# Optimization experiments

Measured on AMD Instinct MI355X. Metric: run time of the kernel, lower is better.

## Reference

```python
import jax, jax.numpy as jnp
import numpy as np

B, T, H, A = 16, 6000, 256, 1
NOTE_CLS = 104            # note_num + 4
NOTE_NUM, NOTE_START = 100, 30
THRESHOLD = 0.5
MIN_GAP = 9


def conv1d(x, w, b):
    # x: [B,T,C], w: [K,Cin,Cout] (kernel 3, padding 1 == SAME)
    return jax.lax.conv_general_dilated(x, w, (1,), 'SAME', dimension_numbers=('NWC', 'WIO', 'NWC')) + b


def layer_norm(x, g, b, eps=1e-5):
    m = jnp.mean(x, -1, keepdims=True)
    v = jnp.mean((x - m) ** 2, -1, keepdims=True)
    return (x - m) * jax.lax.rsqrt(v + eps) * g + b


def regulate_boundary(bd_logits, non_padding):
    # threshold -> per-run local argmax -> min-gap NMS merge, sequential per row
    probs = jax.nn.sigmoid(bd_logits)          # [B,T]
    bd = probs > THRESHOLD
    Tn = probs.shape[1]

    def one_row(bd_i, p_i):
        def step(carry, j):
            res, start, last, best_i, best_v = carry
            is_one, pj = bd_i[j], p_i[j]
            opening = is_one & (start < 0)
            # running argmax over current run (first-occurrence tie-break like torch.argmax)
            upd = opening | (is_one & (start >= 0) & (pj > best_v))
            best_i = jnp.where(upd, j, best_i)
            best_v = jnp.where(upd, pj, best_v)
            start = jnp.where(opening, j, start)
            close = (~is_one) & (start >= 0)
            merge = close & ((best_i - last) < MIN_GAP) & (last > 0)
            # Python round() / half-to-even, matches round((bd_idx+last)/2)
            mid = jnp.round((best_i + last).astype(jnp.float32) * 0.5).astype(jnp.int32)
            final_idx = jnp.where(merge, mid, best_i)
            res = res.at[last].set(jnp.where(merge, 0, res[last]))
            res = res.at[final_idx].set(jnp.where(close, 1, res[final_idx]))
            last = jnp.where(close, final_idx, last)
            start = jnp.where(close, jnp.int32(-1), start)
            return (res, start, last, best_i, best_v), None

        init = (jnp.zeros((Tn,), jnp.int32), jnp.int32(-1), jnp.int32(-1), jnp.int32(0), jnp.float32(-1e30))
        (res, *_), _ = jax.lax.scan(step, init, jnp.arange(Tn, dtype=jnp.int32))
        return res

    res = jax.vmap(one_row)(bd, probs)
    res = res.at[:, 0].set(0)
    lens = non_padding.sum(1)                  # bd_res[i, sum(non_padding[i])-1:] = 0
    res = jnp.where(jnp.arange(Tn)[None, :] >= (lens - 1)[:, None], 0, res)
    return res


def setup_inputs() -> dict:
    key = jax.random.key(0)
    ks = jax.random.split(key, 16)
    s = 1.0 / np.sqrt(H)
    return {
        'feat': jax.random.normal(ks[0], (B, T, H), jnp.float32),
        'non_padding': jnp.ones((B, T), jnp.int32),
        'w_bd': jax.random.normal(ks[1], (H, 1), jnp.float32) * s,
        'b_bd': jnp.zeros((1,), jnp.float32),
        'w_attn': jax.random.normal(ks[2], (H, A), jnp.float32) * s,
        'b_attn': jnp.zeros((A,), jnp.float32),
        'conv_w': jax.random.normal(ks[3], (3, H, H), jnp.float32) * s,
        'conv_b': jnp.zeros((H,), jnp.float32),
        'ln_g': jnp.ones((H,), jnp.float32),
        'ln_b': jnp.zeros((H,), jnp.float32),
        'post_w': jax.random.normal(ks[4], (3, H, H), jnp.float32) * s,
        'post_b': jnp.zeros((H,), jnp.float32),
        'w_pitch': jax.random.normal(ks[5], (H, NOTE_CLS), jnp.float32) * s,
        'b_pitch': jnp.zeros((NOTE_CLS,), jnp.float32),
    }


def reference(feat, non_padding, w_bd, b_bd, w_attn, b_attn, conv_w, conv_b, ln_g, ln_b, post_w, post_b, w_pitch, b_pitch):
    # note boundary logits (note_bd_out, temperature 1, clamp)
    note_bd_logits = jnp.clip((feat @ w_bd + b_bd)[..., 0], -16.0, 16.0)      # [B,T]
    note_bd = regulate_boundary(note_bd_logits, non_padding)                  # [B,T] int

    # --- PitchDecoder ---
    attn = jax.nn.sigmoid(feat @ w_attn + b_attn)                             # [B,T,A]
    attn_mean = attn.mean(-1)                                                 # [B,T]
    # mean over heads of feat[...,None]*attn[:,:,None,:] == feat * mean(attn)
    attn_feat = feat * attn_mean[..., None]                                   # [B,T,H]
    mel2note = jnp.cumsum(note_bd, axis=1)                                    # [B,T]
    note_lengths = note_bd.sum(axis=1) + 1
    N = feat.shape[1] + 1                                                     # static upper bound on note_length
    seg = jax.vmap(lambda d, s2: jax.ops.segment_sum(d, s2, num_segments=N))
    denom = seg(attn_mean, mel2note)                                          # [B,N]
    agg = seg(attn_feat, mel2note) / (denom[..., None] + 1e-5)                # [B,N,H]
    # post ConvBlocks (1 residual conv layer + post conv, kernel 3, leakyrelu)
    h = jax.nn.leaky_relu(layer_norm(conv1d(agg, conv_w, conv_b), ln_g, ln_b), 0.01)
    agg = conv1d(agg + h, post_w, post_b)
    note_logits = agg @ w_pitch + b_pitch                                     # [B,N,104]
    note_pred = jnp.argmax(note_logits, axis=-1)
    note_pred = jnp.where((note_pred > NOTE_NUM) | (note_pred < NOTE_START), 0, note_pred)
    return note_bd_logits, note_bd, note_lengths, note_logits, note_pred
```

## Files before the change

kernel.cpp:

```cpp
#include <hip/hip_runtime.h>
#include <math.h>

#define B 16
#define T 6000
#define H 256
#define NPOS 6001
#define NOTE_CLS 104
#define NOTE_NUM 100
#define NOTE_START 30
#define MIN_GAP 9
#define SEGC 384

#define T2 16
#define NT2 ((NPOS + T2 - 1) / T2)
#define CT 4
#define NCT (SEGC / CT)
#define ZSTR 260

#define NWORDS 94
#define MAXRUNS 3088

__global__ __launch_bounds__(256) void k_dots(
    const float* __restrict__ feat,
    const float* __restrict__ w_bd, const float* __restrict__ b_bd,
    const float* __restrict__ w_attn, const float* __restrict__ b_attn,
    float* __restrict__ out_logits, double* __restrict__ dlog,
    float* __restrict__ amean)
{
  int lane = threadIdx.x & 63, wv = threadIdx.x >> 6;
  int row = blockIdx.x * 4 + wv;
  if (row >= B * T) return;
  float4 f  = ((const float4*)(feat + (size_t)row * H))[lane];
  float4 wb = ((const float4*)w_bd)[lane];
  float4 wa = ((const float4*)w_attn)[lane];
  double sb = (double)f.x * wb.x + (double)f.y * wb.y + (double)f.z * wb.z + (double)f.w * wb.w;
  double sa = (double)f.x * wa.x + (double)f.y * wa.y + (double)f.z * wa.z + (double)f.w * wa.w;
  for (int off = 32; off; off >>= 1) { sb += __shfl_down(sb, off); sa += __shfl_down(sa, off); }
  if (lane == 0) {
    double lb = sb + (double)b_bd[0];
    lb = fmin(fmax(lb, -16.0), 16.0);
    out_logits[row] = (float)lb;
    dlog[row] = lb;
    double la = sa + (double)b_attn[0];
    amean[row] = (float)(1.0 / (1.0 + exp(-la)));
  }
}

__device__ __forceinline__ int block_scan_excl(int* a, int n, int tid, int lane,
                                               int wv, int* wsums)
{
  int base = 0;
  for (int c0 = 0; c0 < n; c0 += 256) {
    int i = c0 + tid;
    int v = (i < n) ? a[i] : 0;
    int s = v;
    #pragma unroll
    for (int off = 1; off < 64; off <<= 1) {
      int t = __shfl_up(s, off);
      if (lane >= off) s += t;
    }
    if (lane == 63) wsums[wv] = s;
    __syncthreads();
    int wbase = 0;
    for (int w = 0; w < wv; ++w) wbase += wsums[w];
    int ctot = wsums[0] + wsums[1] + wsums[2] + wsums[3];
    if (i < n) a[i] = base + wbase + s - v;
    base += ctot;
    __syncthreads();
  }
  return base;
}

__global__ __launch_bounds__(256) void k_regulate(
    const double* __restrict__ dlog, const int* __restrict__ non_padding,
    float* __restrict__ out_bd, float* __restrict__ out_len,
    int* __restrict__ seg_start, int* __restrict__ note_len)
{
  __shared__ double row_s[T];
  __shared__ unsigned long long words[96];
  __shared__ unsigned long long smask[NWORDS], emask[NWORDS];
  __shared__ int wcnt[NWORDS], woff[NWORDS], ecnt[NWORDS], eoff[NWORDS];
  __shared__ int starts_s[MAXRUNS];
  __shared__ int ends_s[MAXRUNS];
  __shared__ int besti_s[MAXRUNS];
  __shared__ int cstart_s[MAXRUNS + 1];
  __shared__ int kofs_s[MAXRUNS];
  __shared__ unsigned long long cmask[52];
  __shared__ int ccnt[52], coff[52];
  __shared__ int wsums[4], red_i[4];
  __shared__ int R_s, NC_s, lens_s;

  int b = blockIdx.x, tid = threadIdx.x;
  int lane = tid & 63, wv = tid >> 6;
  const double* row = dlog + (size_t)b * T;

  for (int c = 0; c < 24; ++c) {
    int t = c * 256 + tid;
    double d = (t < T) ? row[t] : -1.0;
    if (t < T) row_s[t] = d;
    unsigned long long m = __ballot((t < T) && (d > 0.0));
    if (lane == 0) words[c * 4 + wv] = m;
  }
  __syncthreads();

  if (tid < NWORDS) {
    unsigned long long bits = words[tid];
    unsigned long long carry = (tid > 0) ? (words[tid - 1] >> 63) : 0ull;
    unsigned long long pm = (bits << 1) | carry;
    unsigned long long sm = bits & ~pm;
    unsigned long long em = (~bits) & pm;
    smask[tid] = sm;  emask[tid] = em;
    wcnt[tid] = __popcll(sm);  ecnt[tid] = __popcll(em);
  }
  __syncthreads();

  if (tid == 0) {
    int a = 0, e = 0;
    #pragma unroll 8
    for (int w = 0; w < NWORDS; ++w) {
      woff[w] = a; a += wcnt[w];
      eoff[w] = e; e += ecnt[w];
    }
    R_s = a;
  }
  __syncthreads();

  if (tid < NWORDS) {
    unsigned long long m = smask[tid];
    int off = woff[tid], base = tid * 64;
    while (m) { int i = __builtin_ctzll(m); starts_s[off++] = base + i; m &= m - 1; }
    m = emask[tid]; off = eoff[tid];
    while (m) { int i = __builtin_ctzll(m); ends_s[off++] = base + i; m &= m - 1; }
  }

  {
    int lens = 0;
    const int* npr = non_padding + (size_t)b * T;
    for (int t = tid; t < T; t += 256) lens += npr[t];
    for (int off = 32; off; off >>= 1) lens += __shfl_down(lens, off);
    if (lane == 0) red_i[wv] = lens;
  }
  __syncthreads();
  if (tid == 0) lens_s = red_i[0] + red_i[1] + red_i[2] + red_i[3];

  int R = R_s;
  int bd_last = (int)((words[(T - 1) >> 6] >> ((T - 1) & 63)) & 1ull);
  int Rc = R - (bd_last ? 1 : 0);

  for (int r = tid; r < R; r += 256) {
    int s = starts_s[r];
    int e = (r < Rc) ? ends_s[r] : T;
    double bv = row_s[s];
    int bi = s;
    for (int t = s + 1; t < e; ++t) {
      double d = row_s[t];
      if (d > bv) { bv = d; bi = t; }
    }
    besti_s[r] = bi;
  }
  __syncthreads();

  int NRW = (Rc + 63) >> 6;
  for (int c0 = 0; c0 < NRW * 64; c0 += 256) {
    int r = c0 + tid;
    bool fl = false;
    if (r < Rc) fl = (r == 0) || (besti_s[r] - besti_s[r - 1] >= MIN_GAP);
    unsigned long long m = __ballot(fl);
    int widx = (c0 >> 6) + wv;
    if (lane == 0 && widx < 52) cmask[widx] = m;
  }
  __syncthreads();
  if (tid < NRW) ccnt[tid] = __popcll(cmask[tid]);
  __syncthreads();
  if (tid == 0) {
    int a = 0;
    for (int w = 0; w < NRW; ++w) { coff[w] = a; a += ccnt[w]; }
    NC_s = a;
  }
  __syncthreads();
  if (tid < NRW) {
    unsigned long long m = cmask[tid];
    int off = coff[tid], base = tid * 64;
    while (m) { int i = __builtin_ctzll(m); cstart_s[off++] = base + i; m &= m - 1; }
  }
  __syncthreads();
  int NC = NC_s;
  if (tid == 0) cstart_s[NC] = Rc;
  __syncthreads();

  for (int j = tid; j < NC; j += 256) {
    int r0 = cstart_s[j], r1 = cstart_s[j + 1];
    int last = -1, kc = 0;
    for (int r = r0; r < r1; ++r) {
      int bi = besti_s[r];
      bool merge = (last > 0) && (bi - last < MIN_GAP);
      int fi = bi;
      if (merge) { int sm2 = bi + last; fi = (sm2 + ((sm2 >> 1) & 1)) >> 1; }
      if (merge) besti_s[r0 + kc - 1] = fi;
      else       besti_s[r0 + kc++]   = fi;
      last = fi;
    }
    kofs_s[j] = kc;
  }
  __syncthreads();

  int K = block_scan_excl(kofs_s, NC, tid, lane, wv, wsums);
  __syncthreads();
  for (int j = tid; j < NC; j += 256) {
    int off = kofs_s[j];
    int cnt = ((j + 1 < NC) ? kofs_s[j + 1] : K) - off;
    int src = cstart_s[j];
    for (int k = 0; k < cnt; ++k) starts_s[off + k] = besti_s[src + k];
  }
  __syncthreads();

  int lens = lens_s;
  for (int i = tid; i < K; i += 256) {
    int e = starts_s[i];
    ends_s[i] = (e != 0 && e < lens - 1) ? 1 : 0;
  }
  __syncthreads();
  int keep = block_scan_excl(ends_s, K, tid, lane, wv, wsums);

  float* obd = out_bd + (size_t)b * T;
  for (int t = tid; t < T; t += 256) obd[t] = 0.f;
  __syncthreads();
  int* ss = seg_start + b * (T + 2);
  for (int i = tid; i < K; i += 256) {
    int e = starts_s[i];
    if (e != 0 && e < lens - 1) {
      int pos = ends_s[i];
      ss[pos + 1] = e;
      obd[e] = 1.f;
    }
  }
  if (tid == 0) {
    ss[0] = 0;
    ss[keep + 1] = T;
    note_len[b] = keep + 1;
    out_len[b] = (float)(keep + 1);
  }
}

__global__ __launch_bounds__(256) void k_consts(
    const float* __restrict__ conv_b, const float* __restrict__ ln_g,
    const float* __restrict__ ln_b, const float* __restrict__ post_w,
    const float* __restrict__ post_b, const float* __restrict__ w_pitch,
    const float* __restrict__ b_pitch,
    float* __restrict__ lmid, float* __restrict__ ledge, int* __restrict__ preds)
{
  __shared__ float hc[H], zm[H], ze[H], red[8];
  __shared__ float lm[NOTE_CLS], le[NOTE_CLS];
  int tid = threadIdx.x, lane = tid & 63, wv = tid >> 6;
  float y = conv_b[tid];
  float s = y;
  for (int off = 32; off; off >>= 1) s += __shfl_down(s, off);
  if (lane == 0) red[wv] = s;
  __syncthreads();
  float mean = (red[0] + red[1] + red[2] + red[3]) * (1.0f / H);
  float d = y - mean, q = d * d;
  for (int off = 32; off; off >>= 1) q += __shfl_down(q, off);
  if (lane == 0) red[4 + wv] = q;
  __syncthreads();
  float var = (red[4] + red[5] + red[6] + red[7]) * (1.0f / H);
  float h = d / sqrtf(var + 1e-5f) * ln_g[tid] + ln_b[tid];
  h = h > 0.f ? h : 0.01f * h;
  hc[tid] = h;
  __syncthreads();
  float am = 0.f, ae = 0.f;
  for (int cin = 0; cin < H; ++cin) {
    float hv = hc[cin];
    float p0 = post_w[(0 * H + cin) * H + tid];
    float p1 = post_w[(1 * H + cin) * H + tid];
    float p2 = post_w[(2 * H + cin) * H + tid];
    am += (p0 + p1 + p2) * hv;
    ae += (p0 + p1) * hv;
  }
  zm[tid] = am + post_b[tid];
  ze[tid] = ae + post_b[tid];
  __syncthreads();
  if (tid < NOTE_CLS) {
    float sm = 0.f, se = 0.f;
    for (int c = 0; c < H; ++c) {
      float w = w_pitch[c * NOTE_CLS + tid];
      sm += zm[c] * w; se += ze[c] * w;
    }
    lm[tid] = sm + b_pitch[tid]; le[tid] = se + b_pitch[tid];
    lmid[tid] = lm[tid]; ledge[tid] = le[tid];
  }
  __syncthreads();
  if (tid == 0) {
    int bi = 0; float bv = lm[0];
    for (int p = 1; p < NOTE_CLS; ++p) if (lm[p] > bv) { bv = lm[p]; bi = p; }
    preds[0] = (bi > NOTE_NUM || bi < NOTE_START) ? 0 : bi;
    bi = 0; bv = le[0];
    for (int p = 1; p < NOTE_CLS; ++p) if (le[p] > bv) { bv = le[p]; bi = p; }
    preds[1] = (bi > NOTE_NUM || bi < NOTE_START) ? 0 : bi;
  }
}

__global__ __launch_bounds__(64) void k_seg(
    const float* __restrict__ feat, const float* __restrict__ amean,
    const int* __restrict__ seg_start, const int* __restrict__ note_len,
    float* __restrict__ agg)
{
  int blk = blockIdx.x;
  int b = blk / SEGC, n = blk - b * SEGC;
  int len = note_len[b];
  int lane = threadIdx.x;
  float4* o4 = (float4*)(agg + ((size_t)b * SEGC + n) * H);
  if (n >= len) {
    if (n < len + 40) o4[lane] = make_float4(0.f, 0.f, 0.f, 0.f);
    return;
  }
  int s = seg_start[b * (T + 2) + n];
  int e = seg_start[b * (T + 2) + n + 1];
  float4 acc = make_float4(0.f, 0.f, 0.f, 0.f);
  float dsum = 0.f;
  for (int t = s; t < e; ++t) {
    float am = amean[(size_t)b * T + t];
    float4 f = ((const float4*)(feat + ((size_t)b * T + t) * H))[lane];
    acc.x += am * f.x; acc.y += am * f.y; acc.z += am * f.z; acc.w += am * f.w;
    dsum += am;
  }
  float dn = dsum + 1e-5f;
  acc.x /= dn; acc.y /= dn; acc.z /= dn; acc.w /= dn;
  o4[lane] = acc;
}

__device__ __forceinline__ void conv_ranges(int len, int& Nz, int& MY)
{
  int t16 = ((len + 2) / 16) * 16;
  if (t16 > SEGC - 16) t16 = SEGC - 16;
  Nz = t16 + 16;
  MY = Nz + 2;
  if (MY > NPOS) MY = NPOS;
  if (MY > SEGC) MY = SEGC;
}

__global__ __launch_bounds__(256) void k_conv1u(
    const float* __restrict__ agg,
    const float* __restrict__ conv_w, const float* __restrict__ conv_b,
    const float* __restrict__ ln_g, const float* __restrict__ ln_b,
    const int* __restrict__ note_len,
    float* __restrict__ u_buf)
{
  int blk = blockIdx.x;
  int b = blk / NCT, tile = blk - b * NCT;
  int t0 = tile * CT;
  int len = note_len[b];
  int Nz, MY;
  conv_ranges(len, Nz, MY);
  if (t0 >= MY) return;

  __shared__ float xs[H][8];
  __shared__ float rs_[CT][4], rq_[CT][4];
  __shared__ float smean[CT], srstd[CT];

  int tid = threadIdx.x;
  int lane = tid & 63, wv = tid >> 6;
  const float* aggb = agg + (size_t)b * SEGC * H;

  #pragma unroll
  for (int r = 0; r < 6; ++r) {
    int p = t0 - 1 + r;
    float v = 0.f;
    if (p >= 0 && p < SEGC) v = aggb[(size_t)p * H + tid];
    xs[tid][r] = v;
  }
  xs[tid][6] = 0.f; xs[tid][7] = 0.f;
  __syncthreads();

  float acc[CT];
  #pragma unroll
  for (int j = 0; j < CT; ++j) acc[j] = 0.f;
  #pragma unroll 4
  for (int cin = 0; cin < H; ++cin) {
    float w0 = conv_w[cin * H + tid];
    float w1 = conv_w[(H + cin) * H + tid];
    float w2 = conv_w[(2 * H + cin) * H + tid];
    float4 X = *(const float4*)&xs[cin][0];
    float2 Y = *(const float2*)&xs[cin][4];
    float L[6] = { X.x, X.y, X.z, X.w, Y.x, Y.y };
    #pragma unroll
    for (int j = 0; j < CT; ++j)
      acc[j] += w0 * L[j] + w1 * L[j + 1] + w2 * L[j + 2];
  }
  {
    float cb = conv_b[tid];
    #pragma unroll
    for (int j = 0; j < CT; ++j) acc[j] += cb;
  }

  #pragma unroll 1
  for (int j = 0; j < CT; ++j) {
    float s = acc[j], q = acc[j] * acc[j];
    for (int off = 32; off; off >>= 1) { s += __shfl_down(s, off); q += __shfl_down(q, off); }
    if (lane == 0) { rs_[j][wv] = s; rq_[j][wv] = q; }
  }
  __syncthreads();
  if (tid < CT) {
    float S = rs_[tid][0] + rs_[tid][1] + rs_[tid][2] + rs_[tid][3];
    float Q = rq_[tid][0] + rq_[tid][1] + rq_[tid][2] + rq_[tid][3];
    float mean = S * (1.0f / H);
    float var = Q * (1.0f / H) - mean * mean;
    if (var < 0.f) var = 0.f;
    smean[tid] = mean;
    srstd[tid] = 1.0f / sqrtf(var + 1e-5f);
  }
  __syncthreads();

  float g = ln_g[tid], bb = ln_b[tid];
  float* ub = u_buf + (size_t)b * SEGC * H;
  #pragma unroll
  for (int j = 0; j < CT; ++j) {
    int m = t0 + j;
    if (m < MY) {
      float h = (acc[j] - smean[j]) * srstd[j] * g + bb;
      h = h > 0.f ? h : 0.01f * h;
      ub[(size_t)m * H + tid] = xs[tid][j + 1] + h;
    }
  }
}

__global__ __launch_bounds__(256) void k_conv2p(
    const float* __restrict__ u_buf,
    const float* __restrict__ post_w, const float* __restrict__ post_b,
    const float* __restrict__ w_pitch, const float* __restrict__ b_pitch,
    const int* __restrict__ note_len,
    float* __restrict__ out3, float* __restrict__ out4)
{
  int blk = blockIdx.x;
  int b = blk / NCT, tile = blk - b * NCT;
  int t0 = tile * CT;
  int len = note_len[b];
  if ((t0 & ~15) > len + 2) return;
  int Nz, MY;
  conv_ranges(len, Nz, MY);

  __shared__ float us_[H][8];
  __shared__ float zt[CT * ZSTR];
  __shared__ float pvs[CT][26];
  __shared__ int   pis[CT][26];

  int tid = threadIdx.x;
  const float* ub = u_buf + (size_t)b * SEGC * H;

  #pragma unroll
  for (int r = 0; r < 6; ++r) {
    int m = t0 - 1 + r;
    float v = 0.f;
    if (m >= 0 && m < MY) v = ub[(size_t)m * H + tid];
    us_[tid][r] = v;
  }
  us_[tid][6] = 0.f; us_[tid][7] = 0.f;
  __syncthreads();

  float acc[CT];
  #pragma unroll
  for (int j = 0; j < CT; ++j) acc[j] = 0.f;
  #pragma unroll 4
  for (int cin = 0; cin < H; ++cin) {
    float w0 = post_w[cin * H + tid];
    float w1 = post_w[(H + cin) * H + tid];
    float w2 = post_w[(2 * H + cin) * H + tid];
    float4 X = *(const float4*)&us_[cin][0];
    float2 Y = *(const float2*)&us_[cin][4];
    float L[6] = { X.x, X.y, X.z, X.w, Y.x, Y.y };
    #pragma unroll
    for (int j = 0; j < CT; ++j)
      acc[j] += w0 * L[j] + w1 * L[j + 1] + w2 * L[j + 2];
  }
  {
    float pb = post_b[tid];
    #pragma unroll
    for (int j = 0; j < CT; ++j) zt[j * ZSTR + tid] = acc[j] + pb;
  }
  __syncthreads();

  if (tid < 104) {
    int n8 = tid / 26, c26 = tid - n8 * 26;
    float4 a = make_float4(0.f, 0.f, 0.f, 0.f);
    const float* z = &zt[n8 * ZSTR];
    #pragma unroll 4
    for (int cin = 0; cin < H; ++cin) {
      float4 w4 = *(const float4*)&w_pitch[cin * NOTE_CLS + 4 * c26];
      float zv = z[cin];
      a.x += zv * w4.x; a.y += zv * w4.y; a.z += zv * w4.z; a.w += zv * w4.w;
    }
    float4 bp = *(const float4*)&b_pitch[4 * c26];
    a.x += bp.x; a.y += bp.y; a.z += bp.z; a.w += bp.w;
    int n = t0 + n8;
    if (n < NPOS)
      *(float4*)&out3[((size_t)b * NPOS + n) * NOTE_CLS + 4 * c26] = a;
    float bv = a.x; int bi = 4 * c26;
    if (a.y > bv) { bv = a.y; bi = 4 * c26 + 1; }
    if (a.z > bv) { bv = a.z; bi = 4 * c26 + 2; }
    if (a.w > bv) { bv = a.w; bi = 4 * c26 + 3; }
    pvs[n8][c26] = bv; pis[n8][c26] = bi;
  }
  __syncthreads();
  if (tid < CT && t0 + tid < NPOS) {
    float bv = pvs[tid][0]; int bi = pis[tid][0];
    #pragma unroll 1
    for (int k = 1; k < 26; ++k)
      if (pvs[tid][k] > bv) { bv = pvs[tid][k]; bi = pis[tid][k]; }
    int pred = (bi > NOTE_NUM || bi < NOTE_START) ? 0 : bi;
    out4[(size_t)b * NPOS + t0 + tid] = (float)pred;
  }
}

__global__ __launch_bounds__(256) void k_tail(
    const float* __restrict__ lmid, const float* __restrict__ ledge,
    const int* __restrict__ preds, const int* __restrict__ note_len,
    float* __restrict__ out3, float* __restrict__ out4)
{
  int blk = blockIdx.x;
  int b = blk / NT2, tile = blk - b * NT2;
  int t0 = tile * T2;
  int len = note_len[b];
  if (t0 <= len + 2) return;
  __shared__ float lm[NOTE_CLS], le[NOTE_CLS];
  int tid = threadIdx.x;
  if (tid < NOTE_CLS) { lm[tid] = lmid[tid]; le[tid] = ledge[tid]; }
  __syncthreads();
  int pm = preds[0], pe = preds[1];
  for (int i = tid; i < T2 * NOTE_CLS; i += 256) {
    int dn = i / NOTE_CLS;
    int n = t0 + dn, p = i - dn * NOTE_CLS;
    if (n >= NPOS) continue;
    out3[((size_t)b * NPOS + n) * NOTE_CLS + p] = (n == NPOS - 1) ? le[p] : lm[p];
  }
  if (tid < T2) {
    int n = t0 + tid;
    if (n < NPOS) out4[(size_t)b * NPOS + n] = (float)((n == NPOS - 1) ? pe : pm);
  }
}

extern "C" void kernel_launch(void* const* d_in, const int* in_sizes, int n_in,
                              void* d_out, int out_size, void* d_ws, size_t ws_size,
                              hipStream_t stream) {
  (void)in_sizes; (void)n_in; (void)out_size; (void)ws_size;
  const float* feat    = (const float*)d_in[0];
  const int*   nonpad  = (const int*)d_in[1];
  const float* w_bd    = (const float*)d_in[2];
  const float* b_bd    = (const float*)d_in[3];
  const float* w_attn  = (const float*)d_in[4];
  const float* b_attn  = (const float*)d_in[5];
  const float* conv_w  = (const float*)d_in[6];
  const float* conv_b  = (const float*)d_in[7];
  const float* ln_g    = (const float*)d_in[8];
  const float* ln_b    = (const float*)d_in[9];
  const float* post_w  = (const float*)d_in[10];
  const float* post_b  = (const float*)d_in[11];
  const float* w_pitch = (const float*)d_in[12];
  const float* b_pitch = (const float*)d_in[13];

  float* out  = (float*)d_out;
  float* out0 = out;
  float* out1 = out + (size_t)B * T;
  float* out2 = out + 2ull * B * T;
  float* out3 = out2 + B;
  float* out4 = out3 + (size_t)B * NPOS * NOTE_CLS;

  char* ws = (char*)d_ws;
  double* dlog  = (double*)(ws + 0);
  float*  amean = (float*)(ws + 768000);
  int*    segst = (int*)(ws + 1152000);
  int*    nlen  = (int*)(ws + 1536128);
  float*  lmid  = (float*)(ws + 1536192);
  float*  ledge = (float*)(ws + 1536608);
  int*    preds = (int*)(ws + 1537024);
  float*  agg   = (float*)(ws + 1537536);
  float*  u_buf = (float*)(ws + 1537536 + 6291456);

  k_dots<<<(B * T) / 4, 256, 0, stream>>>(feat, w_bd, b_bd, w_attn, b_attn, out0, dlog, amean);
  k_regulate<<<B, 256, 0, stream>>>(dlog, nonpad, out1, out2, segst, nlen);
  k_consts<<<1, 256, 0, stream>>>(conv_b, ln_g, ln_b, post_w, post_b, w_pitch, b_pitch, lmid, ledge, preds);
  k_seg<<<B * SEGC, 64, 0, stream>>>(feat, amean, segst, nlen, agg);
  k_conv1u<<<B * NCT, 256, 0, stream>>>(agg, conv_w, conv_b, ln_g, ln_b, nlen, u_buf);
  k_conv2p<<<B * NCT, 256, 0, stream>>>(u_buf, post_w, post_b, w_pitch, b_pitch, nlen, out3, out4);
  k_tail<<<B * NT2, 256, 0, stream>>>(lmid, ledge, preds, nlen, out3, out4);
}
```

Measured before the change: 282.4 us.

## Split post conv and pitch projection into separate larger-tile kernels

Replaces the fused post-conv plus pitch-projection kernel with two kernels. The conv kernel now computes 16-position tiles per output-channel group, with each thread accumulating 8 positions, to improve weight reuse. Its results go to a new global buffer, and a separate 416-thread kernel computes the pitch logits and argmax for 16 rows at a time. It also raises the unroll factor in the first conv loop. The cost is an extra kernel launch and a global round trip through the new buffer, which needs more workspace.

```diff
diff --git a/kernel.cpp b/kernel.cpp
--- a/kernel.cpp
+++ b/kernel.cpp
@@ -15,6 +15,7 @@
 #define NT2 ((NPOS + T2 - 1) / T2)
 #define CT 4
 #define NCT (SEGC / CT)
+#define NT16 (SEGC / 16)
 #define ZSTR 260
 
 #define NWORDS 94
@@ -374,7 +375,7 @@
   float acc[CT];
   #pragma unroll
   for (int j = 0; j < CT; ++j) acc[j] = 0.f;
-  #pragma unroll 4
+  #pragma unroll 8
   for (int cin = 0; cin < H; ++cin) {
     float w0 = conv_w[cin * H + tid];
     float w1 = conv_w[(H + cin) * H + tid];
@@ -423,65 +424,92 @@
   }
 }
 
-__global__ __launch_bounds__(256) void k_conv2p(
+__global__ __launch_bounds__(128) void k_conv2z(
     const float* __restrict__ u_buf,
     const float* __restrict__ post_w, const float* __restrict__ post_b,
+    const int* __restrict__ note_len,
+    float* __restrict__ zbuf)
+{
+  int blk = blockIdx.x;
+  int b = blk / (NT16 * 4);
+  int rem = blk - b * (NT16 * 4);
+  int tile = rem >> 2, cg = rem & 3;
+  int t0 = tile * 16;
+  int len = note_len[b];
+  if (t0 > len + 2) return;
+  int Nz, MY;
+  conv_ranges(len, Nz, MY);
+
+  __shared__ float us[H][20];
+
+  int tid = threadIdx.x;
+  int cout = (tid & 63) + (cg << 6);
+  int ph = tid >> 6;
+  const float* ub = u_buf + (size_t)b * SEGC * H;
+
+  for (int r = 0; r < 18; ++r) {
+    int m = t0 - 1 + r;
+    bool ok = (m >= 0 && m < MY);
+    for (int c = tid; c < H; c += 128)
+      us[c][r] = ok ? ub[(size_t)m * H + c] : 0.f;
+  }
+  __syncthreads();
+
+  float acc[8];
+  #pragma unroll
+  for (int j = 0; j < 8; ++j) acc[j] = 0.f;
+  #pragma unroll 4
+  for (int cin = 0; cin < H; ++cin) {
+    float w0 = post_w[cin * H + cout];
+    float w1 = post_w[(H + cin) * H + cout];
+    float w2 = post_w[(2 * H + cin) * H + cout];
+    const float* rowp = &us[cin][ph * 8];
+    float4 X = *(const float4*)&rowp[0];
+    float4 Y = *(const float4*)&rowp[4];
+    float2 Zv = *(const float2*)&rowp[8];
+    float L[10] = { X.x, X.y, X.z, X.w, Y.x, Y.y, Y.z, Y.w, Zv.x, Zv.y };
+    #pragma unroll
+    for (int j = 0; j < 8; ++j)
+      acc[j] += w0 * L[j] + w1 * L[j + 1] + w2 * L[j + 2];
+  }
+  float pb = post_b[cout];
+  float* zb = zbuf + (size_t)b * SEGC * H;
+  #pragma unroll
+  for (int j = 0; j < 8; ++j) {
+    int n = t0 + ph * 8 + j;
+    zb[(size_t)n * H + cout] = acc[j] + pb;
+  }
+}
+
+__global__ __launch_bounds__(416) void k_pitch(
+    const float* __restrict__ zbuf,
     const float* __restrict__ w_pitch, const float* __restrict__ b_pitch,
     const int* __restrict__ note_len,
     float* __restrict__ out3, float* __restrict__ out4)
 {
   int blk = blockIdx.x;
-  int b = blk / NCT, tile = blk - b * NCT;
-  int t0 = tile * CT;
+  int b = blk / NT16, tile = blk - b * NT16;
+  int t0 = tile * 16;
   int len = note_len[b];
-  if ((t0 & ~15) > len + 2) return;
-  int Nz, MY;
-  conv_ranges(len, Nz, MY);
-
-  __shared__ float us_[H][8];
-  __shared__ float zt[CT * ZSTR];
-  __shared__ float pvs[CT][26];
-  __shared__ int   pis[CT][26];
+  if (t0 > len + 2) return;
+
+  __shared__ float zt[16 * ZSTR];
+  __shared__ float pvs[16][26];
+  __shared__ int   pis[16][26];
 
   int tid = threadIdx.x;
-  const float* ub = u_buf + (size_t)b * SEGC * H;
-
-  #pragma unroll
-  for (int r = 0; r < 6; ++r) {
-    int m = t0 - 1 + r;
-    float v = 0.f;
-    if (m >= 0 && m < MY) v = ub[(size_t)m * H + tid];
-    us_[tid][r] = v;
-  }
-  us_[tid][6] = 0.f; us_[tid][7] = 0.f;
-  __syncthreads();
-
-  float acc[CT];
-  #pragma unroll
-  for (int j = 0; j < CT; ++j) acc[j] = 0.f;
-  #pragma unroll 4
-  for (int cin = 0; cin < H; ++cin) {
-    float w0 = post_w[cin * H + tid];
-    float w1 = post_w[(H + cin) * H + tid];
-    float w2 = post_w[(2 * H + cin) * H + tid];
-    float4 X = *(const float4*)&us_[cin][0];
-    float2 Y = *(const float2*)&us_[cin][4];
-    float L[6] = { X.x, X.y, X.z, X.w, Y.x, Y.y };
-    #pragma unroll
-    for (int j = 0; j < CT; ++j)
-      acc[j] += w0 * L[j] + w1 * L[j + 1] + w2 * L[j + 2];
-  }
+  const float* zb = zbuf + (size_t)b * SEGC * H;
+
+  for (int i = tid; i < 16 * H; i += 416) {
+    int n = i >> 8, c = i & 255;
+    zt[n * ZSTR + c] = zb[(size_t)(t0 + n) * H + c];
+  }
+  __syncthreads();
+
   {
-    float pb = post_b[tid];
-    #pragma unroll
-    for (int j = 0; j < CT; ++j) zt[j * ZSTR + tid] = acc[j] + pb;
-  }
-  __syncthreads();
-
-  if (tid < 104) {
-    int n8 = tid / 26, c26 = tid - n8 * 26;
+    int n16 = tid / 26, c26 = tid - n16 * 26;
     float4 a = make_float4(0.f, 0.f, 0.f, 0.f);
-    const float* z = &zt[n8 * ZSTR];
+    const float* z = &zt[n16 * ZSTR];
     #pragma unroll 4
     for (int cin = 0; cin < H; ++cin) {
       float4 w4 = *(const float4*)&w_pitch[cin * NOTE_CLS + 4 * c26];
@@ -490,17 +518,17 @@
     }
     float4 bp = *(const float4*)&b_pitch[4 * c26];
     a.x += bp.x; a.y += bp.y; a.z += bp.z; a.w += bp.w;
-    int n = t0 + n8;
+    int n = t0 + n16;
     if (n < NPOS)
       *(float4*)&out3[((size_t)b * NPOS + n) * NOTE_CLS + 4 * c26] = a;
     float bv = a.x; int bi = 4 * c26;
     if (a.y > bv) { bv = a.y; bi = 4 * c26 + 1; }
     if (a.z > bv) { bv = a.z; bi = 4 * c26 + 2; }
     if (a.w > bv) { bv = a.w; bi = 4 * c26 + 3; }
-    pvs[n8][c26] = bv; pis[n8][c26] = bi;
-  }
-  __syncthreads();
-  if (tid < CT && t0 + tid < NPOS) {
+    pvs[n16][c26] = bv; pis[n16][c26] = bi;
+  }
+  __syncthreads();
+  if (tid < 16 && t0 + tid < NPOS) {
     float bv = pvs[tid][0]; int bi = pis[tid][0];
     #pragma unroll 1
     for (int k = 1; k < 26; ++k)
@@ -573,12 +601,14 @@
   int*    preds = (int*)(ws + 1537024);
   float*  agg   = (float*)(ws + 1537536);
   float*  u_buf = (float*)(ws + 1537536 + 6291456);
+  float*  zbuf  = (float*)(ws + 1537536 + 2 * 6291456);
 
   k_dots<<<(B * T) / 4, 256, 0, stream>>>(feat, w_bd, b_bd, w_attn, b_attn, out0, dlog, amean);
   k_regulate<<<B, 256, 0, stream>>>(dlog, nonpad, out1, out2, segst, nlen);
   k_consts<<<1, 256, 0, stream>>>(conv_b, ln_g, ln_b, post_w, post_b, w_pitch, b_pitch, lmid, ledge, preds);
   k_seg<<<B * SEGC, 64, 0, stream>>>(feat, amean, segst, nlen, agg);
   k_conv1u<<<B * NCT, 256, 0, stream>>>(agg, conv_w, conv_b, ln_g, ln_b, nlen, u_buf);
-  k_conv2p<<<B * NCT, 256, 0, stream>>>(u_buf, post_w, post_b, w_pitch, b_pitch, nlen, out3, out4);
+  k_conv2z<<<B * NT16 * 4, 128, 0, stream>>>(u_buf, post_w, post_b, nlen, zbuf);
+  k_pitch<<<B * NT16, 416, 0, stream>>>(zbuf, w_pitch, b_pitch, nlen, out3, out4);
   k_tail<<<B * NT2, 256, 0, stream>>>(lmid, ledge, preds, nlen, out3, out4);
 }
```

New measurement: 313.0 us. +10.8%, slower.
